# Optimization experiments

Measured on AMD Instinct MI355X. Metric: run time of the kernel, lower is better.

Reference implementation:

```python
import jax, jax.numpy as jnp
import numpy as np

K = 5            # spline kernel size per dim
NUM_CLASSES = 10
EPS = 1e-4       # matches module's normalize eps
ROUTING_ITERS = 3
_BITS = jnp.array([[(b >> 2) & 1, (b >> 1) & 1, b & 1] for b in range(8)], dtype=jnp.float32)  # [8,3]


def normalize(t, axis=-1):
    return t / (jnp.sqrt(jnp.sum(t * t, axis=axis, keepdims=True)) + EPS)


def quat_mul(q, r):
    # quaternions stored (x, y, z, w) -- module sets identity as [:,:,:,3]=1
    qx, qy, qz, qw = q[..., 0], q[..., 1], q[..., 2], q[..., 3]
    rx, ry, rz, rw = r[..., 0], r[..., 1], r[..., 2], r[..., 3]
    return jnp.stack([
        qw * rx + qx * rw + qy * rz - qz * ry,
        qw * ry - qx * rz + qy * rw + qz * rx,
        qw * rz + qx * ry - qy * rx + qz * rw,
        qw * rw - qx * rx - qy * ry - qz * rz,
    ], axis=-1)


def spline_conv(x, pseudo, src, dst, W, root, bias, n_nodes):
    # degree-1 open B-spline conv, kernel 5^3, in=1, out=16
    v = pseudo * (K - 1)                                   # [E,3]
    i0 = jnp.clip(jnp.floor(v), 0, K - 2)                  # [E,3]
    frac = v - i0
    i0 = i0.astype(jnp.int32)
    idx = i0[:, None, :] + _BITS.astype(jnp.int32)[None]   # [E,8,3]
    kflat = (idx[..., 0] * K + idx[..., 1]) * K + idx[..., 2]  # [E,8]
    wb = jnp.prod(jnp.where(_BITS[None] > 0, frac[:, None, :], 1.0 - frac[:, None, :]), axis=-1)  # [E,8]
    Wg = W[kflat]                                          # [E,8,16] irregular gather (dominant traffic)
    wk = jnp.einsum('eb,ebo->eo', wb, Wg)                  # [E,16]
    msg = x[src] * wk                                      # [E,16] (in-channels = 1)
    agg = jax.ops.segment_sum(msg, dst, num_segments=n_nodes)
    deg = jax.ops.segment_sum(jnp.ones_like(dst, dtype=x.dtype), dst, num_segments=n_nodes)
    return agg / jnp.maximum(deg, 1.0)[:, None] + x @ root + bias


def caps_layer(pose, act, q):
    # pose [N,I,4], act [N,I], q [I,J,4] -> pose [N,J,4], act [N,J]
    qn = normalize(q)
    pred = normalize(quat_mul(qn[None], pose[:, :, None, :]))  # [N,I,J,4]
    b = jnp.zeros(pred.shape[:3], dtype=pose.dtype)
    for _ in range(ROUTING_ITERS):
        c = jax.nn.softmax(b, axis=2) * act[:, :, None]
        s = jnp.einsum('nij,nijq->njq', c, pred)
        v = normalize(s)
        b = b + jnp.einsum('nijq,njq->nij', pred, v)
    act_out = jax.nn.sigmoid(jnp.einsum('nij,nijq,njq->nj', c, pred, v))
    return v, act_out


def pool_by_agreement(pose, act, pos, G, start, size):
    # voxel-grid clustering + agreement-weighted quaternion averaging
    g = jnp.clip(jnp.floor((pos - start) / size), 0, G - 1).astype(jnp.int32)  # [N,3]
    vid = (g[:, 0] * G + g[:, 1]) * G + g[:, 2]
    V = G ** 3
    s = jax.ops.segment_sum(act[:, :, None] * pose, vid, num_segments=V)  # [V,J,4]
    m = normalize(s)
    agree = jnp.sum(pose * m[vid], axis=-1)                                # [N,J]
    wsum = jax.ops.segment_sum(act, vid, num_segments=V)
    cnt = jax.ops.segment_sum(jnp.ones((pose.shape[0],), pose.dtype), vid, num_segments=V)
    act_out = jax.nn.sigmoid(jax.ops.segment_sum(act * agree, vid, num_segments=V) / (wsum + EPS))
    pos_out = jax.ops.segment_sum(pos, vid, num_segments=V) / (cnt[:, None] + EPS)
    return m, act_out, pos_out


def forward(x, pos, pseudo, W_spline, root, bias, lin_w, lin_b, q0, q1, q3, q5, q6, q7, edge_index):
    N = x.shape[0]
    src, dst = edge_index[0], edge_index[1]
    h = spline_conv(x, pseudo, src, dst, W_spline, root, bias, N)   # [N,16]
    quats = jax.nn.elu(h) @ lin_w + lin_b                           # [N,4]
    pose = normalize(quats.reshape(N, 1, 4))                        # [N,1,4]
    act = x.reshape(N, 1)                                           # expand to num_caps_in=1
    pose, act = caps_layer(pose, act, q0)                           # 1 -> 6
    pose, act = caps_layer(pose, act, q1)                           # 6 -> 6
    min_pos, max_pos = pos.min(), pos.max()
    rng = max_pos + 0.001 - min_pos
    pose, act, p = pool_by_agreement(pose, act, pos, 32, min_pos, rng / 32)   # -> 32768 voxels
    pose, act = caps_layer(pose, act, q3)                           # 6 -> 8
    pose, act, p = pool_by_agreement(pose, act, p, 8, min_pos, rng / 8)       # -> 512
    pose, act = caps_layer(pose, act, q5)                           # 8 -> 12
    pose, act, p = pool_by_agreement(pose, act, p, 2, min_pos, rng / 2)       # -> 8
    pose, act = caps_layer(pose, act, q6)                           # 12 -> 14
    pose, act, p = pool_by_agreement(pose, act, p, 1, min_pos - 0.5, max_pos - min_pos + 1.0)  # -> 1
    pose, act = caps_layer(pose, act, q7)                           # 14 -> 10
    return act                                                      # [1, 10]


def setup_inputs() -> dict:
    key = jax.random.key(0)
    ks = jax.random.split(key, 16)
    N, E = 50000, 800000
    def caps_q(k, i, j):
        return jax.random.normal(k, (i, j, 4), dtype=jnp.float32)
    return {
        'x': jax.random.uniform(ks[0], (N, 1), dtype=jnp.float32),
        'pos': jax.random.uniform(ks[1], (N, 3), dtype=jnp.float32),
        'pseudo': jax.random.uniform(ks[2], (E, 3), dtype=jnp.float32),
        'W_spline': jax.random.normal(ks[3], (K ** 3, 16), dtype=jnp.float32) * 0.1,
        'root': jax.random.normal(ks[4], (1, 16), dtype=jnp.float32) * 0.1,
        'bias': jnp.zeros((16,), dtype=jnp.float32),
        'lin_w': jax.random.normal(ks[5], (16, 4), dtype=jnp.float32) * 0.25,
        'lin_b': jnp.zeros((4,), dtype=jnp.float32),
        'q0': caps_q(ks[6], 1, 6),
        'q1': caps_q(ks[7], 6, 6),
        'q3': caps_q(ks[8], 6, 8),
        'q5': caps_q(ks[9], 8, 12),
        'q6': caps_q(ks[10], 12, 14),
        'q7': caps_q(ks[11], 14, NUM_CLASSES),
        'edge_index': jax.random.randint(ks[12], (2, E), 0, N, dtype=jnp.int32),
    }


def reference(x, pos, pseudo, W_spline, root, bias, lin_w, lin_b, q0, q1, q3, q5, q6, q7, edge_index):
    return forward(x, pos, pseudo, W_spline, root, bias, lin_w, lin_b, q0, q1, q3, q5, q6, q7, edge_index)
```

## Files before the change

### kernel.cpp

```cpp
#include <hip/hip_runtime.h>
#include <math.h>

#define EPS 1e-4f

__device__ __forceinline__ float sigmoidf_(float x){ return 1.0f/(1.0f+expf(-x)); }

__device__ __forceinline__ unsigned f2u_(float f){
    unsigned u = __float_as_uint(f);
    return (u & 0x80000000u) ? ~u : (u | 0x80000000u);
}
__device__ __forceinline__ float u2f_(unsigned u){
    unsigned b = (u & 0x80000000u) ? (u & 0x7FFFFFFFu) : ~u;
    return __uint_as_float(b);
}

__global__ void minmax_kernel(const float* __restrict__ p, int n, unsigned* mm){
    float lo = INFINITY, hi = -INFINITY;
    for (int i = blockIdx.x*blockDim.x + threadIdx.x; i < n; i += gridDim.x*blockDim.x){
        float v = p[i]; lo = fminf(lo, v); hi = fmaxf(hi, v);
    }
    for (int off = 32; off > 0; off >>= 1){
        lo = fminf(lo, __shfl_down(lo, off));
        hi = fmaxf(hi, __shfl_down(hi, off));
    }
    __shared__ float slo[8], shi[8];
    int wid = threadIdx.x >> 6;
    if ((threadIdx.x & 63) == 0){ slo[wid] = lo; shi[wid] = hi; }
    __syncthreads();
    if (threadIdx.x == 0){
        int nw = blockDim.x >> 6;
        for (int w = 1; w < nw; w++){ lo = fminf(lo, slo[w]); hi = fmaxf(hi, shi[w]); }
        atomicMin(&mm[0], f2u_(lo));
        atomicMax(&mm[1], f2u_(hi));
    }
}

__global__ void elist_edge(const int* __restrict__ ei, int* __restrict__ head,
                           int* __restrict__ nxt, int E, int N){
    int e = blockIdx.x*blockDim.x + threadIdx.x;
    if (e >= E) return;
    int d = ei[E + e];
    nxt[e] = atomicExch(&head[(e & 3)*N + d], e);
}

__device__ __forceinline__ int voxel_id(const float* __restrict__ pos, int n, int G,
                                        float start, float size){
    int g[3];
    #pragma unroll
    for (int k = 0; k < 3; k++){
        float gg = floorf((pos[(size_t)n*3 + k] - start) / size);
        gg = fminf(fmaxf(gg, 0.f), (float)(G - 1));
        g[k] = (int)gg;
    }
    return (g[0]*G + g[1])*G + g[2];
}

__device__ __forceinline__ void pool_geom(const unsigned* mm, int G, int mode,
                                          float& start, float& size){
    float mn = u2f_(mm[0]), mx = u2f_(mm[1]);
    if (mode == 0){ start = mn; size = (mx + 0.001f - mn) / (float)G; }
    else          { start = mn - 0.5f; size = mx - mn + 1.0f; }
}

__global__ void elist_node(const float* __restrict__ pos, int* __restrict__ head,
                           int* __restrict__ nxt, int N, int G, int mode,
                           const unsigned* __restrict__ mm){
    int n = blockIdx.x*blockDim.x + threadIdx.x;
    if (n >= N) return;
    float start, size; pool_geom(mm, G, mode, start, size);
    int v = voxel_id(pos, n, G, start, size);
    nxt[n] = atomicExch(&head[v], n);
}

__global__ __launch_bounds__(256)
void spline_node_kernel(const float* __restrict__ x, const float* __restrict__ pseudo,
                        const int* __restrict__ ei,
                        const int* __restrict__ head, const int* __restrict__ nxt,
                        const float* __restrict__ W,
                        const float* __restrict__ root, const float* __restrict__ bias,
                        const float* __restrict__ lin_w, const float* __restrict__ lin_b,
                        float* __restrict__ pose, float* __restrict__ act, int N, int E){
    __shared__ float Ws[125*17];
    for (int i = threadIdx.x; i < 125*16; i += blockDim.x)
        Ws[(i >> 4)*17 + (i & 15)] = W[i];
    __syncthreads();
    int t = blockIdx.x*blockDim.x + threadIdx.x;
    int n = t >> 2;
    int k = t & 3;
    if (n >= N) return;

    float agg[16];
    #pragma unroll
    for (int o = 0; o < 16; o++) agg[o] = 0.f;

    int cnt = 0;
    for (int e = head[k*N + n]; e >= 0; e = nxt[e]){
        float p0 = pseudo[3*e], p1 = pseudo[3*e+1], p2 = pseudo[3*e+2];
        float xv = x[ei[e]];
        float v0 = p0*4.f, v1 = p1*4.f, v2 = p2*4.f;
        float f0 = fminf(fmaxf(floorf(v0), 0.f), 3.f);
        float f1 = fminf(fmaxf(floorf(v1), 0.f), 3.f);
        float f2 = fminf(fmaxf(floorf(v2), 0.f), 3.f);
        float fr0 = v0 - f0, fr1 = v1 - f1, fr2 = v2 - f2;
        int i0 = (int)f0, i1 = (int)f1, i2 = (int)f2;
        #pragma unroll
        for (int b = 0; b < 8; b++){
            int b0 = (b >> 2) & 1, b1 = (b >> 1) & 1, b2 = b & 1;
            float w = (b0 ? fr0 : 1.f - fr0) * (b1 ? fr1 : 1.f - fr1) * (b2 ? fr2 : 1.f - fr2);
            w *= xv;
            int kk = ((i0 + b0)*5 + (i1 + b1))*5 + (i2 + b2);
            const float* Wr = &Ws[kk*17];
            #pragma unroll
            for (int o = 0; o < 16; o++) agg[o] += w * Wr[o];
        }
        cnt++;
    }

    #pragma unroll
    for (int o = 0; o < 16; o++){
        agg[o] += __shfl_xor(agg[o], 1);
        agg[o] += __shfl_xor(agg[o], 2);
    }
    cnt += __shfl_xor(cnt, 1);
    cnt += __shfl_xor(cnt, 2);

    if (k != 0) return;

    float deg = fmaxf((float)cnt, 1.0f);
    float xs = x[n];
    float qv0 = lin_b[0], qv1 = lin_b[1], qv2 = lin_b[2], qv3 = lin_b[3];
    #pragma unroll
    for (int o = 0; o < 16; o++){
        float h = agg[o] / deg + xs * root[o] + bias[o];
        float e = (h > 0.f) ? h : expm1f(h);
        qv0 += e * lin_w[o*4 + 0];
        qv1 += e * lin_w[o*4 + 1];
        qv2 += e * lin_w[o*4 + 2];
        qv3 += e * lin_w[o*4 + 3];
    }
    float inv = 1.0f / (sqrtf(qv0*qv0 + qv1*qv1 + qv2*qv2 + qv3*qv3) + EPS);
    pose[(size_t)n*4 + 0] = qv0*inv;
    pose[(size_t)n*4 + 1] = qv1*inv;
    pose[(size_t)n*4 + 2] = qv2*inv;
    pose[(size_t)n*4 + 3] = qv3*inv;
    act[n] = xs;
}

template<int I, int J, int NPB>
__global__ __launch_bounds__(NPB*I*J)
void caps_coop_kernel(const float* __restrict__ poseIn, const float* __restrict__ actIn,
                      const float* __restrict__ q, float* __restrict__ poseOut,
                      float* __restrict__ actOut, int N){
    const int IJ = I*J;
    const int tid = threadIdx.x;
    const int nl  = tid / IJ;
    const int li  = tid - nl*IJ;
    const int i   = li / J;
    const int j   = li - i*J;
    const int node = blockIdx.x*NPB + nl;
    const bool on = (node < N);

    __shared__ float redA[NPB][I*J];
    __shared__ float redB[NPB][I*J];
    __shared__ float cp[NPB][I*J*4];
    __shared__ float vsh[NPB][J*4];

    float prx=0.f, pry=0.f, prz=0.f, prw=0.f, ai=0.f;
    if (on){
        float qx = q[li*4+0], qy = q[li*4+1], qz = q[li*4+2], qw = q[li*4+3];
        float qinv = 1.0f/(sqrtf(qx*qx+qy*qy+qz*qz+qw*qw)+EPS);
        qx*=qinv; qy*=qinv; qz*=qinv; qw*=qinv;
        const float* pp = &poseIn[((size_t)node*I + i)*4];
        float rx=pp[0], ry=pp[1], rz=pp[2], rw=pp[3];
        ai = actIn[(size_t)node*I + i];
        float tx = qw*rx + qx*rw + qy*rz - qz*ry;
        float ty = qw*ry - qx*rz + qy*rw + qz*rx;
        float tz = qw*rz + qx*ry - qy*rx + qz*rw;
        float tw = qw*rw - qx*rx - qy*ry - qz*rz;
        float pinv = 1.0f/(sqrtf(tx*tx+ty*ty+tz*tz+tw*tw)+EPS);
        prx=tx*pinv; pry=ty*pinv; prz=tz*pinv; prw=tw*pinv;
    }

    float b = 0.f, c = 0.f;
    for (int t = 0; t < 3; t++){
        redA[nl][li] = b;
        __syncthreads();
        float mb = -INFINITY;
        #pragma unroll
        for (int jj = 0; jj < J; jj++) mb = fmaxf(mb, redA[nl][i*J+jj]);
        float e = expf(b - mb);
        redB[nl][li] = e;
        __syncthreads();
        float s = 0.f;
        #pragma unroll
        for (int jj = 0; jj < J; jj++) s += redB[nl][i*J+jj];
        c = ai * e / s;
        cp[nl][li*4+0] = c*prx; cp[nl][li*4+1] = c*pry;
        cp[nl][li*4+2] = c*prz; cp[nl][li*4+3] = c*prw;
        __syncthreads();
        for (int idx = li; idx < J*4; idx += IJ){
            int jj = idx >> 2, comp = idx & 3;
            float acc = 0.f;
            #pragma unroll
            for (int ii = 0; ii < I; ii++) acc += cp[nl][(ii*J+jj)*4+comp];
            vsh[nl][idx] = acc;
        }
        __syncthreads();
        if (li < J){
            float a0=vsh[nl][li*4], a1=vsh[nl][li*4+1], a2=vsh[nl][li*4+2], a3=vsh[nl][li*4+3];
            float inv = 1.0f/(sqrtf(a0*a0+a1*a1+a2*a2+a3*a3)+EPS);
            vsh[nl][li*4]=a0*inv; vsh[nl][li*4+1]=a1*inv;
            vsh[nl][li*4+2]=a2*inv; vsh[nl][li*4+3]=a3*inv;
        }
        __syncthreads();
        if (t < 2){
            b += prx*vsh[nl][j*4] + pry*vsh[nl][j*4+1] + prz*vsh[nl][j*4+2] + prw*vsh[nl][j*4+3];
            __syncthreads();
        } else {
            redA[nl][li] = c*(prx*vsh[nl][j*4] + pry*vsh[nl][j*4+1]
                            + prz*vsh[nl][j*4+2] + prw*vsh[nl][j*4+3]);
            __syncthreads();
            if (li < J && on){
                float acc = 0.f;
                #pragma unroll
                for (int ii = 0; ii < I; ii++) acc += redA[nl][ii*J+li];
                actOut[(size_t)node*J + li] = sigmoidf_(acc);
                poseOut[((size_t)node*J+li)*4+0] = vsh[nl][li*4+0];
                poseOut[((size_t)node*J+li)*4+1] = vsh[nl][li*4+1];
                poseOut[((size_t)node*J+li)*4+2] = vsh[nl][li*4+2];
                poseOut[((size_t)node*J+li)*4+3] = vsh[nl][li*4+3];
            }
        }
    }
}

template<int J>
__global__ __launch_bounds__(256)
void pool1_gather_kernel(const float* __restrict__ pose, const float* __restrict__ act,
                         const float* __restrict__ pos,
                         const int* __restrict__ head, const int* __restrict__ nxt,
                         float* __restrict__ poseOut, float* __restrict__ actOut,
                         float* __restrict__ posOut, int V){
    int v = blockIdx.x*blockDim.x + threadIdx.x;
    if (v >= V) return;

    float s[J][4], w[J], ps0=0.f, ps1=0.f, ps2=0.f;
    #pragma unroll
    for (int j = 0; j < J; j++){ s[j][0]=0.f; s[j][1]=0.f; s[j][2]=0.f; s[j][3]=0.f; w[j]=0.f; }

    int cnt = 0;
    for (int n = head[v]; n >= 0; n = nxt[n]){
        const float* pb = &pose[(size_t)n*J*4];
        const float* ab = &act[(size_t)n*J];
        #pragma unroll
        for (int j = 0; j < J; j++){
            float aj = ab[j];
            s[j][0] += aj*pb[j*4+0];
            s[j][1] += aj*pb[j*4+1];
            s[j][2] += aj*pb[j*4+2];
            s[j][3] += aj*pb[j*4+3];
            w[j] += aj;
        }
        ps0 += pos[(size_t)n*3+0];
        ps1 += pos[(size_t)n*3+1];
        ps2 += pos[(size_t)n*3+2];
        cnt++;
    }
    #pragma unroll
    for (int j = 0; j < J; j++){
        float inv = 1.0f/(sqrtf(s[j][0]*s[j][0]+s[j][1]*s[j][1]+
                                s[j][2]*s[j][2]+s[j][3]*s[j][3])+EPS);
        s[j][0]*=inv; s[j][1]*=inv; s[j][2]*=inv; s[j][3]*=inv;
    }
    float ag[J];
    #pragma unroll
    for (int j = 0; j < J; j++) ag[j] = 0.f;
    for (int n = head[v]; n >= 0; n = nxt[n]){
        const float* pb = &pose[(size_t)n*J*4];
        const float* ab = &act[(size_t)n*J];
        #pragma unroll
        for (int j = 0; j < J; j++){
            float agree = pb[j*4+0]*s[j][0] + pb[j*4+1]*s[j][1]
                        + pb[j*4+2]*s[j][2] + pb[j*4+3]*s[j][3];
            ag[j] += ab[j]*agree;
        }
    }
    #pragma unroll
    for (int j = 0; j < J; j++){
        size_t o = (size_t)v*J + j;
        actOut[o] = sigmoidf_(ag[j] / (w[j] + EPS));
        poseOut[o*4+0] = s[j][0];
        poseOut[o*4+1] = s[j][1];
        poseOut[o*4+2] = s[j][2];
        poseOut[o*4+3] = s[j][3];
    }
    float c = (float)cnt + EPS;
    posOut[(size_t)v*3+0] = ps0 / c;
    posOut[(size_t)v*3+1] = ps1 / c;
    posOut[(size_t)v*3+2] = ps2 / c;
}

template<int V, int J, int CH, int NCHUNK>
__global__ void pool_priv1(const float4* __restrict__ poseIn, const float* __restrict__ actIn,
                           const float* __restrict__ posIn,
                           float* __restrict__ s, float* __restrict__ wsum,
                           float* __restrict__ cnt, float* __restrict__ psum,
                           int N, int G, int mode, const unsigned* __restrict__ mm){
    __shared__ float s_[V*CH*4];
    __shared__ float wsum_[V*CH];
    __shared__ float cnt_[V];
    __shared__ float psum_[V*3];
    const int chunk = blockIdx.x % NCHUNK;
    const int slice = blockIdx.x / NCHUNK;
    const int nslices = gridDim.x / NCHUNK;
    const int c0 = chunk * CH;

    for (int t = threadIdx.x; t < V*CH*4; t += blockDim.x) s_[t] = 0.f;
    for (int t = threadIdx.x; t < V*CH; t += blockDim.x) wsum_[t] = 0.f;
    if (chunk == 0){
        for (int t = threadIdx.x; t < V; t += blockDim.x) cnt_[t] = 0.f;
        for (int t = threadIdx.x; t < V*3; t += blockDim.x) psum_[t] = 0.f;
    }
    __syncthreads();

    float start, size; pool_geom(mm, G, mode, start, size);
    int per = (N + nslices - 1) / nslices;
    int n0 = slice * per, n1 = min(N, n0 + per);

    for (int n = n0 + (int)threadIdx.x; n < n1; n += blockDim.x){
        int vid = voxel_id(posIn, n, G, start, size);
        #pragma unroll
        for (int jj = 0; jj < CH; jj++){
            int j = c0 + jj;
            float aj = actIn[(size_t)n*J + j];
            float4 p = poseIn[(size_t)n*J + j];
            int b = (vid*CH + jj)*4;
            atomicAdd(&s_[b+0], aj*p.x);
            atomicAdd(&s_[b+1], aj*p.y);
            atomicAdd(&s_[b+2], aj*p.z);
            atomicAdd(&s_[b+3], aj*p.w);
            atomicAdd(&wsum_[vid*CH + jj], aj);
        }
        if (chunk == 0){
            atomicAdd(&cnt_[vid], 1.0f);
            atomicAdd(&psum_[vid*3+0], posIn[(size_t)n*3+0]);
            atomicAdd(&psum_[vid*3+1], posIn[(size_t)n*3+1]);
            atomicAdd(&psum_[vid*3+2], posIn[(size_t)n*3+2]);
        }
    }
    __syncthreads();

    for (int t = threadIdx.x; t < V*CH*4; t += blockDim.x){
        float val = s_[t];
        if (val != 0.f){
            int v = t / (CH*4), r = t % (CH*4);
            atomicAdd(&s[((size_t)v*J + c0)*4 + r], val);
        }
    }
    for (int t = threadIdx.x; t < V*CH; t += blockDim.x){
        float val = wsum_[t];
        if (val != 0.f){
            int v = t / CH, jj = t % CH;
            atomicAdd(&wsum[(size_t)v*J + c0 + jj], val);
        }
    }
    if (chunk == 0){
        for (int t = threadIdx.x; t < V; t += blockDim.x)
            if (cnt_[t] != 0.f) atomicAdd(&cnt[t], cnt_[t]);
        for (int t = threadIdx.x; t < V*3; t += blockDim.x)
            if (psum_[t] != 0.f) atomicAdd(&psum[t], psum_[t]);
    }
}

template<int V, int J>
__global__ void pool_priv2(const float4* __restrict__ poseIn, const float* __restrict__ actIn,
                           const float* __restrict__ posIn, const float4* __restrict__ m,
                           float* __restrict__ agacc,
                           int N, int G, int mode, const unsigned* __restrict__ mm){
    __shared__ float ag_[V*J];
    for (int t = threadIdx.x; t < V*J; t += blockDim.x) ag_[t] = 0.f;
    __syncthreads();
    float start, size; pool_geom(mm, G, mode, start, size);
    int nslices = gridDim.x;
    int per = (N + nslices - 1) / nslices;
    int n0 = blockIdx.x * per, n1 = min(N, n0 + per);
    for (int n = n0 + (int)threadIdx.x; n < n1; n += blockDim.x){
        int vid = voxel_id(posIn, n, G, start, size);
        #pragma unroll
        for (int j = 0; j < J; j++){
            float4 p  = poseIn[(size_t)n*J + j];
            float4 mv = m[(size_t)vid*J + j];
            float agree = p.x*mv.x + p.y*mv.y + p.z*mv.z + p.w*mv.w;
            atomicAdd(&ag_[vid*J + j], actIn[(size_t)n*J + j]*agree);
        }
    }
    __syncthreads();
    for (int t = threadIdx.x; t < V*J; t += blockDim.x)
        if (ag_[t] != 0.f) atomicAdd(&agacc[t], ag_[t]);
}

__global__ void pool_m(const float* __restrict__ s, float* __restrict__ m, int VJ){
    int t = blockIdx.x*blockDim.x + threadIdx.x;
    if (t >= VJ) return;
    float a = s[(size_t)t*4], b = s[(size_t)t*4+1], c = s[(size_t)t*4+2], d = s[(size_t)t*4+3];
    float inv = 1.0f / (sqrtf(a*a + b*b + c*c + d*d) + EPS);
    m[(size_t)t*4]   = a*inv;
    m[(size_t)t*4+1] = b*inv;
    m[(size_t)t*4+2] = c*inv;
    m[(size_t)t*4+3] = d*inv;
}

__global__ void pool_fin(const float* __restrict__ agacc, const float* __restrict__ wsum,
                         const float* __restrict__ cnt, const float* __restrict__ psum,
                         float* __restrict__ actOut, float* __restrict__ posOut, int V, int J){
    int t = blockIdx.x*blockDim.x + threadIdx.x;
    if (t >= V*J) return;
    int v = t / J, j = t % J;
    actOut[t] = sigmoidf_(agacc[t] / (wsum[t] + EPS));
    if (j == 0){
        float c = cnt[v] + EPS;
        posOut[(size_t)v*3 + 0] = psum[(size_t)v*3 + 0] / c;
        posOut[(size_t)v*3 + 1] = psum[(size_t)v*3 + 1] / c;
        posOut[(size_t)v*3 + 2] = psum[(size_t)v*3 + 2] / c;
    }
}

template<int V, int J, int CH>
__global__ void pool_fused_kernel(const float* __restrict__ poseIn, const float* __restrict__ actIn,
                                  const float* __restrict__ posIn,
                                  float* __restrict__ poseOut, float* __restrict__ actOut,
                                  float* __restrict__ posOut,
                                  int N, int G, int mode, const unsigned* __restrict__ mm){
    __shared__ float s_[V*CH*4];
    __shared__ float wsum_[V*CH];
    __shared__ float ag_[V*CH];
    __shared__ float cnt_[V];
    __shared__ float psum_[V*3];
    const int c0 = blockIdx.x * CH;

    for (int t = threadIdx.x; t < V*CH*4; t += blockDim.x) s_[t] = 0.f;
    for (int t = threadIdx.x; t < V*CH; t += blockDim.x){ wsum_[t] = 0.f; ag_[t] = 0.f; }
    if (blockIdx.x == 0){
        for (int t = threadIdx.x; t < V; t += blockDim.x) cnt_[t] = 0.f;
        for (int t = threadIdx.x; t < V*3; t += blockDim.x) psum_[t] = 0.f;
    }
    __syncthreads();

    float start, size; pool_geom(mm, G, mode, start, size);

    for (int n = threadIdx.x; n < N; n += blockDim.x){
        int vid = voxel_id(posIn, n, G, start, size);
        #pragma unroll
        for (int jj = 0; jj < CH; jj++){
            int j = c0 + jj;
            float aj = actIn[(size_t)n*J + j];
            const float* pb = &poseIn[((size_t)n*J + j)*4];
            int b = (vid*CH + jj)*4;
            atomicAdd(&s_[b+0], aj*pb[0]);
            atomicAdd(&s_[b+1], aj*pb[1]);
            atomicAdd(&s_[b+2], aj*pb[2]);
            atomicAdd(&s_[b+3], aj*pb[3]);
            atomicAdd(&wsum_[vid*CH + jj], aj);
        }
        if (blockIdx.x == 0){
            atomicAdd(&cnt_[vid], 1.0f);
            atomicAdd(&psum_[vid*3+0], posIn[(size_t)n*3+0]);
            atomicAdd(&psum_[vid*3+1], posIn[(size_t)n*3+1]);
            atomicAdd(&psum_[vid*3+2], posIn[(size_t)n*3+2]);
        }
    }
    __syncthreads();

    for (int t = threadIdx.x; t < V*CH; t += blockDim.x){
        float a = s_[t*4], b = s_[t*4+1], c = s_[t*4+2], d = s_[t*4+3];
        float inv = 1.0f / (sqrtf(a*a + b*b + c*c + d*d) + EPS);
        s_[t*4] = a*inv; s_[t*4+1] = b*inv; s_[t*4+2] = c*inv; s_[t*4+3] = d*inv;
    }
    __syncthreads();

    for (int n = threadIdx.x; n < N; n += blockDim.x){
        int vid = voxel_id(posIn, n, G, start, size);
        #pragma unroll
        for (int jj = 0; jj < CH; jj++){
            int j = c0 + jj;
            const float* pb = &poseIn[((size_t)n*J + j)*4];
            const float* mb = &s_[(vid*CH + jj)*4];
            float agree = pb[0]*mb[0] + pb[1]*mb[1] + pb[2]*mb[2] + pb[3]*mb[3];
            atomicAdd(&ag_[vid*CH + jj], actIn[(size_t)n*J + j]*agree);
        }
    }
    __syncthreads();

    for (int t = threadIdx.x; t < V*CH; t += blockDim.x){
        int v = t / CH, jj = t % CH;
        size_t o = (size_t)v*J + c0 + jj;
        actOut[o] = sigmoidf_(ag_[t] / (wsum_[t] + EPS));
        poseOut[o*4+0] = s_[t*4+0];
        poseOut[o*4+1] = s_[t*4+1];
        poseOut[o*4+2] = s_[t*4+2];
        poseOut[o*4+3] = s_[t*4+3];
    }
    if (blockIdx.x == 0){
        for (int v = threadIdx.x; v < V; v += blockDim.x){
            float c = cnt_[v] + EPS;
            posOut[(size_t)v*3+0] = psum_[(size_t)v*3+0] / c;
            posOut[(size_t)v*3+1] = psum_[(size_t)v*3+1] / c;
            posOut[(size_t)v*3+2] = psum_[(size_t)v*3+2] / c;
        }
    }
}

extern "C" void kernel_launch(void* const* d_in, const int* in_sizes, int n_in,
                              void* d_out, int out_size, void* d_ws, size_t ws_size,
                              hipStream_t stream){
    const float* x      = (const float*)d_in[0];
    const float* pos    = (const float*)d_in[1];
    const float* pseudo = (const float*)d_in[2];
    const float* Wsp    = (const float*)d_in[3];
    const float* root   = (const float*)d_in[4];
    const float* bias   = (const float*)d_in[5];
    const float* lin_w  = (const float*)d_in[6];
    const float* lin_b  = (const float*)d_in[7];
    const float* q0     = (const float*)d_in[8];
    const float* q1     = (const float*)d_in[9];
    const float* q3     = (const float*)d_in[10];
    const float* q5     = (const float*)d_in[11];
    const float* q6     = (const float*)d_in[12];
    const float* q7     = (const float*)d_in[13];
    const int*   ei     = (const int*)d_in[14];
    const int N = in_sizes[0];
    const int E = in_sizes[2] / 3;
    const int V1 = 32768;

    char* ws = (char*)d_ws;
    size_t off = 0;
    auto alloc = [&](size_t bytes)->void*{
        void* p = ws + off;
        off += (bytes + 255) & ~(size_t)255;
        return p;
    };
    unsigned* mm   = (unsigned*)alloc(8);
    int* ehead     = (int*)alloc((size_t)4*N*sizeof(int));
    int* enxt      = (int*)alloc((size_t)E*sizeof(int));
    int* vhead     = (int*)alloc((size_t)V1*sizeof(int));
    int* vnxt      = (int*)alloc((size_t)N*sizeof(int));
    float* P0  = (float*)alloc((size_t)1250000*sizeof(float));
    float* P1  = (float*)alloc((size_t)1250000*sizeof(float));
    float* A0  = (float*)alloc((size_t)310000*sizeof(float));
    float* A1  = (float*)alloc((size_t)310000*sizeof(float));
    float* PB0 = (float*)alloc((size_t)100000*sizeof(float));
    float* PB1 = (float*)alloc((size_t)100000*sizeof(float));
    size_t pool_off0 = off;
    float* vs  = (float*)alloc((size_t)512*8*4*sizeof(float));
    float* vw  = (float*)alloc((size_t)512*8*sizeof(float));
    float* va  = (float*)alloc((size_t)512*8*sizeof(float));
    float* vc  = (float*)alloc((size_t)512*sizeof(float));
    float* vp  = (float*)alloc((size_t)512*3*sizeof(float));
    size_t pool_bytes = off - pool_off0;

    hipMemsetAsync(mm,     0xFF, 4, stream);
    hipMemsetAsync(mm + 1, 0x00, 4, stream);
    hipMemsetAsync(ehead, 0xFF, (size_t)4*N*sizeof(int), stream);
    hipMemsetAsync(vhead, 0xFF, (size_t)V1*sizeof(int), stream);

    minmax_kernel<<<80, 256, 0, stream>>>(pos, N*3, mm);

    elist_edge<<<(E + 255)/256, 256, 0, stream>>>(ei, ehead, enxt, E, N);
    spline_node_kernel<<<(4*N + 255)/256, 256, 0, stream>>>(x, pseudo, ei, ehead, enxt, Wsp,
                                                            root, bias, lin_w, lin_b, P0, A0, N, E);

    caps_coop_kernel<1,6,32><<<(N + 31)/32, 32*6, 0, stream>>>(P0, A0, q0, P1, A1, N);
    caps_coop_kernel<6,6,7><<<(N + 6)/7, 7*36, 0, stream>>>(P1, A1, q1, P0, A0, N);

    {
        const int G = 32;
        elist_node<<<(N + 255)/256, 256, 0, stream>>>(pos, vhead, vnxt, N, G, 0, mm);
        pool1_gather_kernel<6><<<(V1 + 255)/256, 256, 0, stream>>>(P0, A0, pos, vhead, vnxt,
                                                                   P1, A1, PB0, V1);
    }
    caps_coop_kernel<6,8,5><<<(32768 + 4)/5, 5*48, 0, stream>>>(P1, A1, q3, P0, A0, 32768);

    {
        const int V = 512, J = 8, G = 8, NSL = 64;
        hipMemsetAsync(vs, 0, pool_bytes, stream);
        pool_priv1<V,J,4,2><<<2*NSL, 256, 0, stream>>>((const float4*)P0, A0, PB0,
                                                       vs, vw, vc, vp, 32768, G, 0, mm);
        pool_m<<<(V*J + 255)/256, 256, 0, stream>>>(vs, P1, V*J);
        pool_priv2<V,J><<<NSL, 256, 0, stream>>>((const float4*)P0, A0, PB0,
                                                 (const float4*)P1, va, 32768, G, 0, mm);
        pool_fin<<<(V*J + 255)/256, 256, 0, stream>>>(va, vw, vc, vp, A1, PB1, V, J);
    }
    caps_coop_kernel<8,12,2><<<256, 2*96, 0, stream>>>(P1, A1, q5, P0, A0, 512);

    {
        const int V = 8, J = 12, G = 2, NSL = 16;
        hipMemsetAsync(vs, 0, pool_bytes, stream);
        pool_priv1<V,J,12,1><<<NSL, 256, 0, stream>>>((const float4*)P0, A0, PB1,
                                                      vs, vw, vc, vp, 512, G, 0, mm);
        pool_m<<<1, 256, 0, stream>>>(vs, P1, V*J);
        pool_priv2<V,J><<<NSL, 256, 0, stream>>>((const float4*)P0, A0, PB1,
                                                 (const float4*)P1, va, 512, G, 0, mm);
        pool_fin<<<1, 256, 0, stream>>>(va, vw, vc, vp, A1, PB0, V, J);
    }
    caps_coop_kernel<12,14,1><<<8, 168, 0, stream>>>(P1, A1, q6, P0, A0, 8);

    pool_fused_kernel<1,14,14><<<1, 1024, 0, stream>>>(P0, A0, PB0, P1, A1, PB1, 8, 1, 1, mm);
    caps_coop_kernel<14,10,1><<<1, 140, 0, stream>>>(P1, A1, q7, P0, (float*)d_out, 1);
}
```

Baseline: 335.6 us.

## Pack per-edge spline data into aligned records and widen linked-list split to 8

The edge-list build kernel now precomputes the spline fractions, the source feature value and the base kernel index, and stores them with the next pointer in a 32-byte aligned record per edge. The node kernel then walks each chain with one float4 and one int2 load instead of scattered pseudo, edge-index, x and next-pointer reads. The per-node lists are also split into 8 chains instead of 4, with 8 threads per node, to shorten each serial pointer chase. The cost is more record storage and write traffic in the pack kernel, a larger head array to memset, and twice as many threads, most of which go idle in the epilogue.

```diff
diff --git a/kernel.cpp b/kernel.cpp
--- a/kernel.cpp
+++ b/kernel.cpp
@@ -35,12 +35,24 @@
     }
 }
 
-__global__ void elist_edge(const int* __restrict__ ei, int* __restrict__ head,
-                           int* __restrict__ nxt, int E, int N){
+struct __align__(32) Rec { float fr0, fr1, fr2, xv; int base, nxt, pad0, pad1; };
+
+__global__ void edge_pack(const int* __restrict__ ei, const float* __restrict__ pseudo,
+                          const float* __restrict__ x,
+                          int* __restrict__ head, Rec* __restrict__ rec, int E, int N){
     int e = blockIdx.x*blockDim.x + threadIdx.x;
     if (e >= E) return;
-    int d = ei[E + e];
-    nxt[e] = atomicExch(&head[(e & 3)*N + d], e);
+    float p0 = pseudo[3*e], p1 = pseudo[3*e+1], p2 = pseudo[3*e+2];
+    int s = ei[e], d = ei[E + e];
+    float v0 = p0*4.f, v1 = p1*4.f, v2 = p2*4.f;
+    float f0 = fminf(fmaxf(floorf(v0), 0.f), 3.f);
+    float f1 = fminf(fmaxf(floorf(v1), 0.f), 3.f);
+    float f2 = fminf(fmaxf(floorf(v2), 0.f), 3.f);
+    float4 fv = make_float4(v0 - f0, v1 - f1, v2 - f2, x[s]);
+    *reinterpret_cast<float4*>(&rec[e]) = fv;
+    int base = ((int)f0*5 + (int)f1)*5 + (int)f2;
+    int nx = atomicExch(&head[(e & 7)*N + d], e);
+    *reinterpret_cast<int2*>(&rec[e].base) = make_int2(base, nx);
 }
 
 __device__ __forceinline__ int voxel_id(const float* __restrict__ pos, int n, int G,
@@ -73,20 +85,19 @@
 }
 
 __global__ __launch_bounds__(256)
-void spline_node_kernel(const float* __restrict__ x, const float* __restrict__ pseudo,
-                        const int* __restrict__ ei,
-                        const int* __restrict__ head, const int* __restrict__ nxt,
+void spline_node_kernel(const float* __restrict__ x, const Rec* __restrict__ rec,
+                        const int* __restrict__ head,
                         const float* __restrict__ W,
                         const float* __restrict__ root, const float* __restrict__ bias,
                         const float* __restrict__ lin_w, const float* __restrict__ lin_b,
-                        float* __restrict__ pose, float* __restrict__ act, int N, int E){
+                        float* __restrict__ pose, float* __restrict__ act, int N){
     __shared__ float Ws[125*17];
     for (int i = threadIdx.x; i < 125*16; i += blockDim.x)
         Ws[(i >> 4)*17 + (i & 15)] = W[i];
     __syncthreads();
     int t = blockIdx.x*blockDim.x + threadIdx.x;
-    int n = t >> 2;
-    int k = t & 3;
+    int n = t >> 3;
+    int k = t & 7;
     if (n >= N) return;
 
     float agg[16];
@@ -94,22 +105,18 @@
     for (int o = 0; o < 16; o++) agg[o] = 0.f;
 
     int cnt = 0;
-    for (int e = head[k*N + n]; e >= 0; e = nxt[e]){
-        float p0 = pseudo[3*e], p1 = pseudo[3*e+1], p2 = pseudo[3*e+2];
-        float xv = x[ei[e]];
-        float v0 = p0*4.f, v1 = p1*4.f, v2 = p2*4.f;
-        float f0 = fminf(fmaxf(floorf(v0), 0.f), 3.f);
-        float f1 = fminf(fmaxf(floorf(v1), 0.f), 3.f);
-        float f2 = fminf(fmaxf(floorf(v2), 0.f), 3.f);
-        float fr0 = v0 - f0, fr1 = v1 - f1, fr2 = v2 - f2;
-        int i0 = (int)f0, i1 = (int)f1, i2 = (int)f2;
+    for (int e = head[k*N + n]; e >= 0; ){
+        const Rec* rp = &rec[e];
+        float4 rv = *reinterpret_cast<const float4*>(rp);
+        int2  ri = *reinterpret_cast<const int2*>(&rp->base);
+        e = ri.y;
+        float fr0 = rv.x, fr1 = rv.y, fr2 = rv.z, xv = rv.w;
         #pragma unroll
         for (int b = 0; b < 8; b++){
             int b0 = (b >> 2) & 1, b1 = (b >> 1) & 1, b2 = b & 1;
             float w = (b0 ? fr0 : 1.f - fr0) * (b1 ? fr1 : 1.f - fr1) * (b2 ? fr2 : 1.f - fr2);
             w *= xv;
-            int kk = ((i0 + b0)*5 + (i1 + b1))*5 + (i2 + b2);
-            const float* Wr = &Ws[kk*17];
+            const float* Wr = &Ws[(ri.x + b0*25 + b1*5 + b2)*17];
             #pragma unroll
             for (int o = 0; o < 16; o++) agg[o] += w * Wr[o];
         }
@@ -120,9 +127,11 @@
     for (int o = 0; o < 16; o++){
         agg[o] += __shfl_xor(agg[o], 1);
         agg[o] += __shfl_xor(agg[o], 2);
+        agg[o] += __shfl_xor(agg[o], 4);
     }
     cnt += __shfl_xor(cnt, 1);
     cnt += __shfl_xor(cnt, 2);
+    cnt += __shfl_xor(cnt, 4);
 
     if (k != 0) return;
 
@@ -540,8 +549,8 @@
         return p;
     };
     unsigned* mm   = (unsigned*)alloc(8);
-    int* ehead     = (int*)alloc((size_t)4*N*sizeof(int));
-    int* enxt      = (int*)alloc((size_t)E*sizeof(int));
+    int* ehead     = (int*)alloc((size_t)8*N*sizeof(int));
+    Rec* erec      = (Rec*)alloc((size_t)E*sizeof(Rec));
     int* vhead     = (int*)alloc((size_t)V1*sizeof(int));
     int* vnxt      = (int*)alloc((size_t)N*sizeof(int));
     float* P0  = (float*)alloc((size_t)1250000*sizeof(float));
@@ -560,14 +569,14 @@
 
     hipMemsetAsync(mm,     0xFF, 4, stream);
     hipMemsetAsync(mm + 1, 0x00, 4, stream);
-    hipMemsetAsync(ehead, 0xFF, (size_t)4*N*sizeof(int), stream);
+    hipMemsetAsync(ehead, 0xFF, (size_t)8*N*sizeof(int), stream);
     hipMemsetAsync(vhead, 0xFF, (size_t)V1*sizeof(int), stream);
 
     minmax_kernel<<<80, 256, 0, stream>>>(pos, N*3, mm);
 
-    elist_edge<<<(E + 255)/256, 256, 0, stream>>>(ei, ehead, enxt, E, N);
-    spline_node_kernel<<<(4*N + 255)/256, 256, 0, stream>>>(x, pseudo, ei, ehead, enxt, Wsp,
-                                                            root, bias, lin_w, lin_b, P0, A0, N, E);
+    edge_pack<<<(E + 255)/256, 256, 0, stream>>>(ei, pseudo, x, ehead, erec, E, N);
+    spline_node_kernel<<<(8*N + 255)/256, 256, 0, stream>>>(x, erec, ehead, Wsp,
+                                                            root, bias, lin_w, lin_b, P0, A0, N);
 
     caps_coop_kernel<1,6,32><<<(N + 31)/32, 32*6, 0, stream>>>(P0, A0, q0, P1, A1, N);
     caps_coop_kernel<6,6,7><<<(N + 6)/7, 7*36, 0, stream>>>(P1, A1, q1, P0, A0, N);
```

Measured after the change: 335.0 us. No clear change (-0.2%).
